# Kernel tuning notes

Hardware: AMD Instinct MI355X
Metric: run time of the kernel (lower is better)

## Reference

```python
import jax, jax.numpy as jnp
import numpy as np

N_DATA = 32768
N_CHK = 32768
N = N_DATA + N_CHK          # 65536 nodes
E = 524288                  # edges (before self-loops)
F_IN = 10                   # node_feature_dim
HID = 128                   # hidden_dim
HEADS = 4
C = HID // HEADS            # 32 per-head channels
L = 4                       # num_gnn_layers
EPS_LN = 1e-5


def layer_norm(x, g, b):
    mu = x.mean(-1, keepdims=True)
    var = ((x - mu) ** 2).mean(-1, keepdims=True)
    return (x - mu) * jax.lax.rsqrt(var + EPS_LN) * g + b


def mlp3(x, W1, b1, W2, b2, W3, b3):
    h = jax.nn.relu(x @ W1 + b1)
    h = jax.nn.relu(h @ W2 + b2)
    return h @ W3 + b3


def setup_inputs() -> dict:
    key = jax.random.key(0)
    ks = jax.random.split(key, 32)
    s = 0.02
    inp = {
        'node_features': jax.random.normal(ks[0], (N, F_IN), jnp.float32),
        'edge_index': jax.random.randint(ks[1], (2, E), 0, N, dtype=jnp.int64),
        # node embedding: Linear(F_IN,HID) + LayerNorm
        'W_emb': s * jax.random.normal(ks[2], (F_IN, HID), jnp.float32),
        'b_emb': jnp.zeros((HID,), jnp.float32),
        'ln0_g': jnp.ones((HID,), jnp.float32),
        'ln0_b': jnp.zeros((HID,), jnp.float32),
        # L GATConv layers (stacked): lin weight, att_src/att_dst, bias, post-LN
        'Wg': s * jax.random.normal(ks[3], (L, HID, HID), jnp.float32),
        'att_s': s * jax.random.normal(ks[4], (L, HEADS, C), jnp.float32),
        'att_d': s * jax.random.normal(ks[5], (L, HEADS, C), jnp.float32),
        'bg': jnp.zeros((L, HID), jnp.float32),
        'lng': jnp.ones((L, HID), jnp.float32),
        'lnb': jnp.zeros((L, HID), jnp.float32),
        # policy net
        'pW1': s * jax.random.normal(ks[6], (HID, HID), jnp.float32),
        'pb1': jnp.zeros((HID,), jnp.float32),
        'pW2': s * jax.random.normal(ks[7], (HID, HID // 2), jnp.float32),
        'pb2': jnp.zeros((HID // 2,), jnp.float32),
        'pW3': s * jax.random.normal(ks[8], (HID // 2, 2), jnp.float32),
        'pb3': jnp.zeros((2,), jnp.float32),
        # value net
        'vW1': s * jax.random.normal(ks[9], (HID, HID), jnp.float32),
        'vb1': jnp.zeros((HID,), jnp.float32),
        'vW2': s * jax.random.normal(ks[10], (HID, HID // 2), jnp.float32),
        'vb2': jnp.zeros((HID // 2,), jnp.float32),
        'vW3': s * jax.random.normal(ks[11], (HID // 2, 1), jnp.float32),
        'vb3': jnp.zeros((1,), jnp.float32),
    }
    return inp


def reference(node_features, edge_index, W_emb, b_emb, ln0_g, ln0_b,
              Wg, att_s, att_d, bg, lng, lnb,
              pW1, pb1, pW2, pb2, pW3, pb3,
              vW1, vb1, vW2, vb2, vW3, vb3):
    n = node_features.shape[0]
    # PyG GATConv adds self-loops by default
    loops = jnp.arange(n, dtype=edge_index.dtype)
    ei = jnp.concatenate([edge_index, jnp.stack([loops, loops])], axis=1)
    src, dst = ei[0], ei[1]

    # node embedding (dropout is identity in eval)
    x = jax.nn.relu(layer_norm(node_features @ W_emb + b_emb, ln0_g, ln0_b))

    for l in range(L):
        h = (x @ Wg[l]).reshape(n, HEADS, C)                       # [N,H,C]
        a_s = jnp.einsum('nhc,hc->nh', h, att_s[l])                # [N,H]
        a_d = jnp.einsum('nhc,hc->nh', h, att_d[l])
        alpha = jax.nn.leaky_relu(a_s[src] + a_d[dst], 0.2)        # [E+N,H]
        # segment softmax over destination node per head
        m = jax.ops.segment_max(alpha, dst, num_segments=n)
        alpha = jnp.exp(alpha - m[dst])
        denom = jax.ops.segment_sum(alpha, dst, num_segments=n)
        alpha = alpha / (denom[dst] + 1e-16)
        out = jax.ops.segment_sum(alpha[:, :, None] * h[src], dst,
                                  num_segments=n)                  # [N,H,C]
        out = out.reshape(n, HID) + bg[l]
        x = layer_norm(x + jax.nn.relu(out), lng[l], lnb[l])

    logits = mlp3(x[:N_DATA], pW1, pb1, pW2, pb2, pW3, pb3)        # [N_DATA,2]
    pooled = x.mean(axis=0, keepdims=True)                         # [1,HID]
    value = mlp3(pooled, vW1, vb1, vW2, vb2, vW3, vb3)             # [1,1]
    return logits, value
```

## Files before the change

kernel.cpp:

```cpp
#include <hip/hip_runtime.h>

#define NNODES 65536
#define NDATA  32768
#define HID    128
#define HEADS  4
#define CHANS  32
#define LAYERS 4

using bf16x8 = __attribute__((ext_vector_type(8))) short;
using f32x4  = __attribute__((ext_vector_type(4))) float;

__device__ __forceinline__ float wave_reduce_sum(float v) {
#pragma unroll
    for (int m = 1; m < 64; m <<= 1) v += __shfl_xor(v, m, 64);
    return v;
}

__device__ __forceinline__ unsigned short bf16_rne(float f) {
    unsigned u = __float_as_uint(f);
    return (unsigned short)((u + 0x7fffu + ((u >> 16) & 1u)) >> 16);
}
__device__ __forceinline__ float bf2f(unsigned short u) {
    return __uint_as_float((unsigned)u << 16);
}

__device__ __forceinline__ void gload_lds16(const unsigned short* g, unsigned short* l) {
    __builtin_amdgcn_global_load_lds(
        (const __attribute__((address_space(1))) void*)g,
        (__attribute__((address_space(3))) void*)l, 16, 0, 0);
}

__global__ void hist_kernel(const int* __restrict__ ei, int* __restrict__ deg, int Eo) {
    int e = blockIdx.x * 256 + threadIdx.x;
    if (e >= Eo) return;
    atomicAdd(&deg[ei[Eo + e]], 1);
}

__global__ void scan1(const int* __restrict__ deg, int* __restrict__ offs, int* __restrict__ bsum) {
    __shared__ int s[256];
    int t = threadIdx.x, b = blockIdx.x;
    int v = deg[b * 256 + t] + 1;
    s[t] = v;
    __syncthreads();
    for (int off = 1; off < 256; off <<= 1) {
        int add = (t >= off) ? s[t - off] : 0;
        __syncthreads();
        s[t] += add;
        __syncthreads();
    }
    offs[b * 256 + t] = s[t] - v;
    if (t == 255) bsum[b] = s[255];
}

__global__ void scan2(int* __restrict__ bsum) {
    __shared__ int s[256];
    int t = threadIdx.x;
    int v = bsum[t];
    s[t] = v;
    __syncthreads();
    for (int off = 1; off < 256; off <<= 1) {
        int add = (t >= off) ? s[t - off] : 0;
        __syncthreads();
        s[t] += add;
        __syncthreads();
    }
    bsum[t] = s[t] - v;
}

__global__ void scan3(int* __restrict__ offs, const int* __restrict__ bsum,
                      int* __restrict__ cursor, int Eo) {
    int i = blockIdx.x * 256 + threadIdx.x;
    int v = offs[i] + bsum[i >> 8];
    offs[i] = v;
    cursor[i] = v;
    if (i == 0) offs[NNODES] = Eo + NNODES;
}

__global__ void fill_kernel(const int* __restrict__ ei, int* __restrict__ cursor,
                            int* __restrict__ col, int Eo) {
    int e = blockIdx.x * 256 + threadIdx.x;
    int Etot = Eo + NNODES;
    if (e >= Etot) return;
    int src, dst;
    if (e < Eo) { src = ei[e]; dst = ei[Eo + e]; }
    else        { src = dst = e - Eo; }
    int pos = atomicAdd(&cursor[dst], 1);
    col[pos] = src;
}

__global__ void prep_all(const float* __restrict__ Wg, const float* __restrict__ attS,
                         const float* __restrict__ attD,
                         const float* __restrict__ pW1, const float* __restrict__ pW2,
                         const float* __restrict__ vW1, const float* __restrict__ vW2,
                         unsigned short* __restrict__ wh, unsigned short* __restrict__ wl,
                         unsigned short* __restrict__ w1h, unsigned short* __restrict__ w1l,
                         unsigned short* __restrict__ w2h, unsigned short* __restrict__ w2l,
                         float* __restrict__ w1t, float* __restrict__ w2t)
{
    int id = blockIdx.x * 256 + threadIdx.x;
    if (id < 4 * 144 * 128) {
        int l = id / (144 * 128);
        int rem = id % (144 * 128);
        int n = rem / 128, k = rem % 128;
        const float* W = Wg + (size_t)l * HID * HID;
        float v = 0.f;
        if (n < 128) {
            v = W[k * HID + n];
        } else if (n < 136) {
            int h = (n - 128) & 3;
            const float* av = ((n - 128) < 4 ? attS : attD) + l * HID + h * CHANS;
            for (int c = 0; c < CHANS; c++) v += W[k * HID + h * CHANS + c] * av[c];
        }
        unsigned short hh = bf16_rne(v);
        int t = n >> 4, bcol = n & 15;
        int ks = k >> 5, kq = (k >> 3) & 3, e = k & 7;
        size_t o = (size_t)l * (144 * 128) + (size_t)(((t * 4 + ks) * 64) + (kq * 16 + bcol)) * 8 + e;
        wh[o] = hh;
        wl[o] = bf16_rne(v - bf2f(hh));
        return;
    }
    id -= 4 * 144 * 128;
    if (id < 24576) {
        int n, k;
        float v;
        unsigned short *dh, *dl;
        if (id < 16384) {
            n = id / 128; k = id % 128;
            v = pW1[k * 128 + n];
            dh = w1h; dl = w1l;
        } else {
            int j = id - 16384;
            n = j / 128; k = j % 128;
            v = pW2[k * 64 + n];
            dh = w2h; dl = w2l;
        }
        unsigned short hh = bf16_rne(v);
        int t = n >> 4, bcol = n & 15;
        int ks = k >> 5, kq = (k >> 3) & 3, e = k & 7;
        size_t o = (size_t)(((t * 4 + ks) * 64) + (kq * 16 + bcol)) * 8 + e;
        dh[o] = hh;
        dl[o] = bf16_rne(v - bf2f(hh));
        return;
    }
    id -= 24576;
    if (id < 16384) {
        int t = id >> 7, k = id & 127;
        w1t[t * 128 + k] = vW1[k * 128 + t];
    } else if (id < 24576) {
        int j = id - 16384;
        int t = j >> 7, k = j & 127;
        w2t[t * 128 + k] = vW2[k * 64 + t];
    }
}

__global__ __launch_bounds__(256) void embed_kernel(
    const float* __restrict__ feat, const float* __restrict__ W,
    const float* __restrict__ bb, const float* __restrict__ g,
    const float* __restrict__ be, unsigned short* __restrict__ xh,
    unsigned short* __restrict__ xl)
{
    int node = blockIdx.x * 4 + (threadIdx.x >> 6);
    int lane = threadIdx.x & 63;
    float f[10];
#pragma unroll
    for (int i = 0; i < 10; i++) f[i] = feat[node * 10 + i];
    int c0 = 2 * lane, c1 = c0 + 1;
    float v0 = bb[c0], v1 = bb[c1];
#pragma unroll
    for (int i = 0; i < 10; i++) {
        v0 = fmaf(f[i], W[i * HID + c0], v0);
        v1 = fmaf(f[i], W[i * HID + c1], v1);
    }
    float mu = wave_reduce_sum(v0 + v1) * (1.f / 128.f);
    float e0 = v0 - mu, e1 = v1 - mu;
    float var = wave_reduce_sum(e0 * e0 + e1 * e1) * (1.f / 128.f);
    float r = 1.f / sqrtf(var + 1e-5f);
    float r0 = fmaxf(e0 * r * g[c0] + be[c0], 0.f);
    float r1 = fmaxf(e1 * r * g[c1] + be[c1], 0.f);
    unsigned short h0 = bf16_rne(r0), h1 = bf16_rne(r1);
    unsigned short l0 = bf16_rne(r0 - bf2f(h0)), l1 = bf16_rne(r1 - bf2f(h1));
    size_t xi = (size_t)node * HID;
    *(unsigned*)(xh + xi + c0) = (unsigned)h0 | ((unsigned)h1 << 16);
    *(unsigned*)(xl + xi + c0) = (unsigned)l0 | ((unsigned)l1 << 16);
}

template <int NT, int EPI>
__global__ __launch_bounds__(512, 4) void mfma_gemm(
    const unsigned short* __restrict__ Ah,
    const unsigned short* __restrict__ Bh, const unsigned short* __restrict__ Bl,
    const float* __restrict__ bias,
    unsigned short* __restrict__ outH,
    float* __restrict__ a_s, float* __restrict__ a_d,
    const float* __restrict__ wfin, const float* __restrict__ bfin,
    float* __restrict__ outF)
{
    __shared__ unsigned short lds[NT * 2048];

    int tid = threadIdx.x;
    int wid = tid >> 6, l = tid & 63;
    int row = blockIdx.x * 128 + wid * 16 + (l & 15);
    int kg = (l >> 4) * 8;

    const unsigned short* arh = Ah + (size_t)row * 128 + kg;
    bf16x8 afh[4];
#pragma unroll
    for (int ks = 0; ks < 4; ks++) afh[ks] = *(const bf16x8*)(arh + ks * 32);

    f32x4 acc[NT];
#pragma unroll
    for (int t = 0; t < NT; t++) acc[t] = (f32x4){0.f, 0.f, 0.f, 0.f};

#pragma unroll
    for (int p = 0; p < 2; p++) {
        __syncthreads();
        for (int c = wid; c < 4 * NT; c += 8) {
            int fr = c >> 1, lo = c & 1;
            int t = fr >> 1, ksl = fr & 1;
            const unsigned short* src = (lo ? Bl : Bh)
                + ((size_t)(t * 4 + p * 2 + ksl) << 9) + ((unsigned)l << 3);
            gload_lds16(src, &lds[(size_t)c << 9]);
        }
        __syncthreads();
#pragma unroll
        for (int ksl = 0; ksl < 2; ksl++) {
            int ks = p * 2 + ksl;
#pragma unroll
            for (int t = 0; t < NT; t++) {
                const unsigned short* bp = &lds[(((t * 2 + ksl) << 1) << 9) + (l << 3)];
                bf16x8 bh  = *(const bf16x8*)bp;
                bf16x8 blo = *(const bf16x8*)(bp + 512);
                acc[t] = __builtin_amdgcn_mfma_f32_16x16x32_bf16(afh[ks], bh,  acc[t], 0, 0, 0);
                acc[t] = __builtin_amdgcn_mfma_f32_16x16x32_bf16(afh[ks], blo, acc[t], 0, 0, 0);
            }
        }
    }

    int ecol = l & 15;
    int er0 = blockIdx.x * 128 + wid * 16 + ((l >> 4) << 2);

    if constexpr (EPI == 0) {
#pragma unroll
        for (int t = 0; t < 8; t++)
#pragma unroll
            for (int j = 0; j < 4; j++)
                outH[(size_t)(er0 + j) * 128 + t * 16 + ecol] = bf16_rne(acc[t][j]);
#pragma unroll
        for (int j = 0; j < 4; j++) {
            float v = acc[8][j];
            if (ecol < 4)      a_s[(er0 + j) * 4 + ecol] = v;
            else if (ecol < 8) a_d[(er0 + j) * 4 + (ecol - 4)] = v;
        }
    } else if constexpr (EPI == 1) {
#pragma unroll
        for (int t = 0; t < NT; t++)
#pragma unroll
            for (int j = 0; j < 4; j++) {
                float v = fmaxf(acc[t][j] + bias[t * 16 + ecol], 0.f);
                outH[(size_t)(er0 + j) * 128 + t * 16 + ecol] = bf16_rne(v);
            }
    } else {
        float p0[4], p1[4];
#pragma unroll
        for (int j = 0; j < 4; j++) { p0[j] = 0.f; p1[j] = 0.f; }
#pragma unroll
        for (int t = 0; t < NT; t++) {
            int cc = t * 16 + ecol;
            float w0 = wfin[cc * 2 + 0], w1 = wfin[cc * 2 + 1];
#pragma unroll
            for (int j = 0; j < 4; j++) {
                float v = fmaxf(acc[t][j] + bias[cc], 0.f);
                p0[j] = fmaf(v, w0, p0[j]);
                p1[j] = fmaf(v, w1, p1[j]);
            }
        }
#pragma unroll
        for (int m = 1; m < 16; m <<= 1)
#pragma unroll
            for (int j = 0; j < 4; j++) {
                p0[j] += __shfl_xor(p0[j], m, 64);
                p1[j] += __shfl_xor(p1[j], m, 64);
            }
        if (ecol == 0) {
            float b0 = bfin[0], b1 = bfin[1];
#pragma unroll
            for (int j = 0; j < 4; j++) {
                outF[(er0 + j) * 2 + 0] = p0[j] + b0;
                outF[(er0 + j) * 2 + 1] = p1[j] + b1;
            }
        }
    }
}

__global__ __launch_bounds__(256) void gat_agg(
    const unsigned short* __restrict__ hb, const float* __restrict__ a_s,
    const float* __restrict__ a_d, const int* __restrict__ offs,
    const int* __restrict__ col, const float* __restrict__ bgl,
    const float* __restrict__ gl, const float* __restrict__ bl,
    unsigned short* __restrict__ xh, unsigned short* __restrict__ xl)
{
    __shared__ int2 whs[4][4][64];
    int wv = threadIdx.x >> 6;
    int lane = threadIdx.x & 63;
    int node = blockIdx.x * 4 + wv;
    int s = offs[node], e = offs[node + 1];
    int deg = e - s;
    float4 ad = *(const float4*)(a_d + (size_t)node * 4);

    int c0 = 2 * lane, c1 = 2 * lane + 1;
    int head = lane >> 4;
    float acc0 = 0.f, acc1 = 0.f;
    float den = 1e-16f;

    if (deg <= 64) {
        int src = 0;
        float e0 = 0.f, e1 = 0.f, e2 = 0.f, e3 = 0.f;
        if (lane < deg) {
            src = col[s + lane];
            float4 as = *(const float4*)(a_s + (size_t)src * 4);
            float s0 = as.x + ad.x; s0 = fmaxf(s0, 0.2f * s0);
            float s1 = as.y + ad.y; s1 = fmaxf(s1, 0.2f * s1);
            float s2 = as.z + ad.z; s2 = fmaxf(s2, 0.2f * s2);
            float s3 = as.w + ad.w; s3 = fmaxf(s3, 0.2f * s3);
            e0 = __expf(s0); e1 = __expf(s1); e2 = __expf(s2); e3 = __expf(s3);
        }
        whs[wv][0][lane] = make_int2(__float_as_int(e0), src);
        whs[wv][1][lane] = make_int2(__float_as_int(e1), src);
        whs[wv][2][lane] = make_int2(__float_as_int(e2), src);
        whs[wv][3][lane] = make_int2(__float_as_int(e3), src);
        const int2* wrow = &whs[wv][head][0];
        int dg4 = (deg + 3) & ~3;
        for (int j = 0; j < dg4; j += 4) {
            int2 q0 = wrow[j + 0], q1 = wrow[j + 1];
            int2 q2 = wrow[j + 2], q3 = wrow[j + 3];
            float w0 = __int_as_float(q0.x), w1 = __int_as_float(q1.x);
            float w2 = __int_as_float(q2.x), w3 = __int_as_float(q3.x);
            unsigned v0 = *(const unsigned*)(hb + (((unsigned)q0.y << 7) + (unsigned)c0));
            unsigned v1 = *(const unsigned*)(hb + (((unsigned)q1.y << 7) + (unsigned)c0));
            unsigned v2 = *(const unsigned*)(hb + (((unsigned)q2.y << 7) + (unsigned)c0));
            unsigned v3 = *(const unsigned*)(hb + (((unsigned)q3.y << 7) + (unsigned)c0));
            den += (w0 + w1) + (w2 + w3);
            acc0 = fmaf(w0, __uint_as_float(v0 << 16), acc0);
            acc1 = fmaf(w0, __uint_as_float(v0 & 0xffff0000u), acc1);
            acc0 = fmaf(w1, __uint_as_float(v1 << 16), acc0);
            acc1 = fmaf(w1, __uint_as_float(v1 & 0xffff0000u), acc1);
            acc0 = fmaf(w2, __uint_as_float(v2 << 16), acc0);
            acc1 = fmaf(w2, __uint_as_float(v2 & 0xffff0000u), acc1);
            acc0 = fmaf(w3, __uint_as_float(v3 << 16), acc0);
            acc1 = fmaf(w3, __uint_as_float(v3 & 0xffff0000u), acc1);
        }
    } else {
        for (int j = s; j < e; j++) {
            int src = col[j];
            float4 as = *(const float4*)(a_s + (size_t)src * 4);
            float sh = (head == 0) ? (as.x + ad.x) : (head == 1) ? (as.y + ad.y)
                     : (head == 2) ? (as.z + ad.z) : (as.w + ad.w);
            sh = fmaxf(sh, 0.2f * sh);
            float wj = __expf(sh);
            den += wj;
            unsigned hv = *(const unsigned*)(hb + (((unsigned)src << 7) + (unsigned)c0));
            acc0 = fmaf(wj, __uint_as_float(hv << 16), acc0);
            acc1 = fmaf(wj, __uint_as_float(hv & 0xffff0000u), acc1);
        }
    }
    float inv = 1.f / den;
    acc0 *= inv;
    acc1 *= inv;

    float o0 = fmaxf(acc0 + bgl[c0], 0.f);
    float o1 = fmaxf(acc1 + bgl[c1], 0.f);
    size_t xi = (size_t)node * HID;
    unsigned ph = *(const unsigned*)(xh + xi + c0);
    unsigned pl = *(const unsigned*)(xl + xi + c0);
    float x0 = __uint_as_float(ph << 16) + __uint_as_float(pl << 16);
    float x1 = __uint_as_float(ph & 0xffff0000u) + __uint_as_float(pl & 0xffff0000u);
    float t0 = x0 + o0, t1 = x1 + o1;
    float mu = wave_reduce_sum(t0 + t1) * (1.f / 128.f);
    float e0 = t0 - mu, e1 = t1 - mu;
    float var = wave_reduce_sum(e0 * e0 + e1 * e1) * (1.f / 128.f);
    float r = 1.f / sqrtf(var + 1e-5f);
    float r0 = e0 * r * gl[c0] + bl[c0];
    float r1 = e1 * r * gl[c1] + bl[c1];
    unsigned short h0 = bf16_rne(r0), h1 = bf16_rne(r1);
    unsigned short l0 = bf16_rne(r0 - bf2f(h0)), l1 = bf16_rne(r1 - bf2f(h1));
    *(unsigned*)(xh + xi + c0) = (unsigned)h0 | ((unsigned)h1 << 16);
    *(unsigned*)(xl + xi + c0) = (unsigned)l0 | ((unsigned)l1 << 16);
}

__global__ void pool_sum(const unsigned short* __restrict__ xh,
                         const unsigned short* __restrict__ xl, float* __restrict__ partial) {
    int t = threadIdx.x;
    int base = blockIdx.x * 256;
    float s = 0.f;
    for (int i = 0; i < 256; i++) {
        size_t idx = (size_t)(base + i) * HID + t;
        s += bf2f(xh[idx]) + bf2f(xl[idx]);
    }
    partial[blockIdx.x * 128 + t] = s;
}

__global__ void value_mlp(const float* __restrict__ partial,
                          const float* __restrict__ w1t, const float* __restrict__ b1,
                          const float* __restrict__ w2t, const float* __restrict__ b2,
                          const float* __restrict__ W3, const float* __restrict__ b3,
                          float* __restrict__ out)
{
    __shared__ float p[128], h1[128], h2[64];
    int t = threadIdx.x;
    float s = 0.f;
    for (int i = 0; i < 256; i++) s += partial[i * 128 + t];
    p[t] = s * (1.f / (float)NNODES);
    __syncthreads();
    float a = b1[t];
    const float4* wr = (const float4*)(w1t + (size_t)t * 128);
#pragma unroll
    for (int k4 = 0; k4 < 32; k4++) {
        float4 w = wr[k4];
        a += p[4 * k4] * w.x + p[4 * k4 + 1] * w.y + p[4 * k4 + 2] * w.z + p[4 * k4 + 3] * w.w;
    }
    h1[t] = fmaxf(a, 0.f);
    __syncthreads();
    if (t < 64) {
        float a2 = b2[t];
        const float4* wr2 = (const float4*)(w2t + (size_t)t * 128);
#pragma unroll
        for (int k4 = 0; k4 < 32; k4++) {
            float4 w = wr2[k4];
            a2 += h1[4 * k4] * w.x + h1[4 * k4 + 1] * w.y + h1[4 * k4 + 2] * w.z + h1[4 * k4 + 3] * w.w;
        }
        h2[t] = fmaxf(a2, 0.f);
    }
    __syncthreads();
    if (t == 0) {
        float v = b3[0];
        for (int k = 0; k < 64; k++) v = fmaf(h2[k], W3[k], v);
        out[NDATA * 2] = v;
    }
}

extern "C" void kernel_launch(void* const* d_in, const int* in_sizes, int n_in,
                              void* d_out, int out_size, void* d_ws, size_t ws_size,
                              hipStream_t stream)
{
    const float* feat  = (const float*)d_in[0];
    const int*   ei    = (const int*)d_in[1];
    const float* W_emb = (const float*)d_in[2];
    const float* b_emb = (const float*)d_in[3];
    const float* ln0g  = (const float*)d_in[4];
    const float* ln0b  = (const float*)d_in[5];
    const float* Wg    = (const float*)d_in[6];
    const float* att_s = (const float*)d_in[7];
    const float* att_d = (const float*)d_in[8];
    const float* bg    = (const float*)d_in[9];
    const float* lng   = (const float*)d_in[10];
    const float* lnb   = (const float*)d_in[11];
    const float* pW1 = (const float*)d_in[12]; const float* pb1 = (const float*)d_in[13];
    const float* pW2 = (const float*)d_in[14]; const float* pb2 = (const float*)d_in[15];
    const float* pW3 = (const float*)d_in[16]; const float* pb3 = (const float*)d_in[17];
    const float* vW1 = (const float*)d_in[18]; const float* vb1 = (const float*)d_in[19];
    const float* vW2 = (const float*)d_in[20]; const float* vb2 = (const float*)d_in[21];
    const float* vW3 = (const float*)d_in[22]; const float* vb3 = (const float*)d_in[23];
    float* out = (float*)d_out;
    int Eo = in_sizes[1] / 2;

    unsigned short* xh = (unsigned short*)d_ws;
    unsigned short* xl = xh + (size_t)NNODES * HID;
    unsigned short* hb = xl + (size_t)NNODES * HID;
    float* a_s = (float*)(hb + (size_t)NNODES * HID);
    float* a_d = a_s + NNODES * HEADS;
    unsigned short* wgt_h = (unsigned short*)(a_d + NNODES * HEADS);
    unsigned short* wgt_l = wgt_h + 4 * 144 * 128;
    unsigned short* pw1h  = wgt_l + 4 * 144 * 128;
    unsigned short* pw1l  = pw1h + 128 * 128;
    unsigned short* pw2h  = pw1l + 128 * 128;
    unsigned short* pw2l  = pw2h + 64 * 128;
    float* w1t  = (float*)(pw2l + 64 * 128);
    float* w2t  = w1t + 128 * 128;
    float* partial = w2t + 64 * 128;
    int* deg    = (int*)(partial + 256 * 128);
    int* offs   = deg + NNODES;
    int* cursor = offs + NNODES + 2;
    int* bsum   = cursor + NNODES;
    int* col    = bsum + 256;
    unsigned short* ph1h = hb;

    prep_all<<<(4 * 144 * 128 + 24576 + 24576) / 256, 256, 0, stream>>>(
        Wg, att_s, att_d, pW1, pW2, vW1, vW2,
        wgt_h, wgt_l, pw1h, pw1l, pw2h, pw2l, w1t, w2t);

    hipMemsetAsync(deg, 0, (size_t)NNODES * 4, stream);
    hist_kernel<<<(Eo + 255) / 256, 256, 0, stream>>>(ei, deg, Eo);
    scan1<<<256, 256, 0, stream>>>(deg, offs, bsum);
    scan2<<<1, 256, 0, stream>>>(bsum);
    scan3<<<256, 256, 0, stream>>>(offs, bsum, cursor, Eo);
    fill_kernel<<<(Eo + NNODES + 255) / 256, 256, 0, stream>>>(ei, cursor, col, Eo);

    embed_kernel<<<NNODES / 4, 256, 0, stream>>>(feat, W_emb, b_emb, ln0g, ln0b, xh, xl);

    for (int l = 0; l < LAYERS; l++) {
        mfma_gemm<9, 0><<<NNODES / 128, 512, 0, stream>>>(
            xh, wgt_h + (size_t)l * 144 * 128, wgt_l + (size_t)l * 144 * 128,
            nullptr, hb, a_s, a_d, nullptr, nullptr, nullptr);
        gat_agg<<<NNODES / 4, 256, 0, stream>>>(
            hb, a_s, a_d, offs, col, bg + l * HID, lng + l * HID, lnb + l * HID, xh, xl);
    }

    mfma_gemm<8, 1><<<NDATA / 128, 512, 0, stream>>>(
        xh, pw1h, pw1l, pb1, ph1h, nullptr, nullptr, nullptr, nullptr, nullptr);
    mfma_gemm<4, 2><<<NDATA / 128, 512, 0, stream>>>(
        ph1h, pw2h, pw2l, pb2, nullptr, nullptr, nullptr, pW3, pb3, out);

    pool_sum<<<256, 128, 0, stream>>>(xh, xl, partial);
    value_mlp<<<1, 128, 0, stream>>>(partial, w1t, vb1, w2t, vb2, vW3, vb3, out);
}
```

Measured before the change: 348.6 us.

## Drop low-bf16 residual storage, fuse embed into prep, merge scan kernels

Node activations are now kept only as a single bf16 array. The low-order residual array xl, along with its reads and writes in gat_agg, embed and pool_sum, is removed, which cuts memory traffic per layer. The embedding kernel is folded into the weight-prep launch, and the separate scan2 block-sum kernel is replaced by a per-block wave reduction inside scan3, removing two launches. In exchange, the residual path and LayerNorm inputs lose precision because they are rounded to bf16 each layer.

New measurement: 330.6 us. 5.2% less time.

```diff
diff --git a/kernel.cpp b/kernel.cpp
--- a/kernel.cpp
+++ b/kernel.cpp
@@ -11,6 +11,12 @@
 using f32x4  = __attribute__((ext_vector_type(4))) float;
 
 __device__ __forceinline__ float wave_reduce_sum(float v) {
+#pragma unroll
+    for (int m = 1; m < 64; m <<= 1) v += __shfl_xor(v, m, 64);
+    return v;
+}
+
+__device__ __forceinline__ int wave_reduce_sum_i(int v) {
 #pragma unroll
     for (int m = 1; m < 64; m <<= 1) v += __shfl_xor(v, m, 64);
     return v;
@@ -52,27 +58,19 @@
     if (t == 255) bsum[b] = s[255];
 }
 
-__global__ void scan2(int* __restrict__ bsum) {
-    __shared__ int s[256];
-    int t = threadIdx.x;
-    int v = bsum[t];
-    s[t] = v;
-    __syncthreads();
-    for (int off = 1; off < 256; off <<= 1) {
-        int add = (t >= off) ? s[t - off] : 0;
-        __syncthreads();
-        s[t] += add;
-        __syncthreads();
-    }
-    bsum[t] = s[t] - v;
-}
-
 __global__ void scan3(int* __restrict__ offs, const int* __restrict__ bsum,
                       int* __restrict__ cursor, int Eo) {
-    int i = blockIdx.x * 256 + threadIdx.x;
-    int v = offs[i] + bsum[i >> 8];
-    offs[i] = v;
-    cursor[i] = v;
+    __shared__ int ws[4];
+    int b = blockIdx.x, t = threadIdx.x;
+    int v = (t < b) ? bsum[t] : 0;
+    v = wave_reduce_sum_i(v);
+    if ((t & 63) == 0) ws[t >> 6] = v;
+    __syncthreads();
+    int base = ws[0] + ws[1] + ws[2] + ws[3];
+    int i = b * 256 + t;
+    int o = offs[i] + base;
+    offs[i] = o;
+    cursor[i] = o;
     if (i == 0) offs[NNODES] = Eo + NNODES;
 }
 
@@ -88,16 +86,43 @@
     col[pos] = src;
 }
 
-__global__ void prep_all(const float* __restrict__ Wg, const float* __restrict__ attS,
-                         const float* __restrict__ attD,
-                         const float* __restrict__ pW1, const float* __restrict__ pW2,
-                         const float* __restrict__ vW1, const float* __restrict__ vW2,
-                         unsigned short* __restrict__ wh, unsigned short* __restrict__ wl,
-                         unsigned short* __restrict__ w1h, unsigned short* __restrict__ w1l,
-                         unsigned short* __restrict__ w2h, unsigned short* __restrict__ w2l,
-                         float* __restrict__ w1t, float* __restrict__ w2t)
+__global__ __launch_bounds__(256) void prep_embed(
+    const float* __restrict__ feat, const float* __restrict__ W_emb,
+    const float* __restrict__ b_emb, const float* __restrict__ ln0g,
+    const float* __restrict__ ln0b, unsigned short* __restrict__ xh,
+    const float* __restrict__ Wg, const float* __restrict__ attS,
+    const float* __restrict__ attD,
+    const float* __restrict__ pW1, const float* __restrict__ pW2,
+    const float* __restrict__ vW1, const float* __restrict__ vW2,
+    unsigned short* __restrict__ wh, unsigned short* __restrict__ wl,
+    unsigned short* __restrict__ w1h, unsigned short* __restrict__ w1l,
+    unsigned short* __restrict__ w2h, unsigned short* __restrict__ w2l,
+    float* __restrict__ w1t, float* __restrict__ w2t)
 {
-    int id = blockIdx.x * 256 + threadIdx.x;
+    if (blockIdx.x < NNODES / 4) {
+        int node = blockIdx.x * 4 + (threadIdx.x >> 6);
+        int lane = threadIdx.x & 63;
+        float f[10];
+#pragma unroll
+        for (int i = 0; i < 10; i++) f[i] = feat[node * 10 + i];
+        int c0 = 2 * lane, c1 = c0 + 1;
+        float v0 = b_emb[c0], v1 = b_emb[c1];
+#pragma unroll
+        for (int i = 0; i < 10; i++) {
+            v0 = fmaf(f[i], W_emb[i * HID + c0], v0);
+            v1 = fmaf(f[i], W_emb[i * HID + c1], v1);
+        }
+        float mu = wave_reduce_sum(v0 + v1) * (1.f / 128.f);
+        float e0 = v0 - mu, e1 = v1 - mu;
+        float var = wave_reduce_sum(e0 * e0 + e1 * e1) * (1.f / 128.f);
+        float r = 1.f / sqrtf(var + 1e-5f);
+        float r0 = fmaxf(e0 * r * ln0g[c0] + ln0b[c0], 0.f);
+        float r1 = fmaxf(e1 * r * ln0g[c1] + ln0b[c1], 0.f);
+        *(unsigned*)(xh + (size_t)node * HID + c0) =
+            (unsigned)bf16_rne(r0) | ((unsigned)bf16_rne(r1) << 16);
+        return;
+    }
+    int id = (blockIdx.x - NNODES / 4) * 256 + threadIdx.x;
     if (id < 4 * 144 * 128) {
         int l = id / (144 * 128);
         int rem = id % (144 * 128);
@@ -153,37 +178,6 @@
     }
 }
 
-__global__ __launch_bounds__(256) void embed_kernel(
-    const float* __restrict__ feat, const float* __restrict__ W,
-    const float* __restrict__ bb, const float* __restrict__ g,
-    const float* __restrict__ be, unsigned short* __restrict__ xh,
-    unsigned short* __restrict__ xl)
-{
-    int node = blockIdx.x * 4 + (threadIdx.x >> 6);
-    int lane = threadIdx.x & 63;
-    float f[10];
-#pragma unroll
-    for (int i = 0; i < 10; i++) f[i] = feat[node * 10 + i];
-    int c0 = 2 * lane, c1 = c0 + 1;
-    float v0 = bb[c0], v1 = bb[c1];
-#pragma unroll
-    for (int i = 0; i < 10; i++) {
-        v0 = fmaf(f[i], W[i * HID + c0], v0);
-        v1 = fmaf(f[i], W[i * HID + c1], v1);
-    }
-    float mu = wave_reduce_sum(v0 + v1) * (1.f / 128.f);
-    float e0 = v0 - mu, e1 = v1 - mu;
-    float var = wave_reduce_sum(e0 * e0 + e1 * e1) * (1.f / 128.f);
-    float r = 1.f / sqrtf(var + 1e-5f);
-    float r0 = fmaxf(e0 * r * g[c0] + be[c0], 0.f);
-    float r1 = fmaxf(e1 * r * g[c1] + be[c1], 0.f);
-    unsigned short h0 = bf16_rne(r0), h1 = bf16_rne(r1);
-    unsigned short l0 = bf16_rne(r0 - bf2f(h0)), l1 = bf16_rne(r1 - bf2f(h1));
-    size_t xi = (size_t)node * HID;
-    *(unsigned*)(xh + xi + c0) = (unsigned)h0 | ((unsigned)h1 << 16);
-    *(unsigned*)(xl + xi + c0) = (unsigned)l0 | ((unsigned)l1 << 16);
-}
-
 template <int NT, int EPI>
 __global__ __launch_bounds__(512, 4) void mfma_gemm(
     const unsigned short* __restrict__ Ah,
@@ -296,7 +290,7 @@
     const float* __restrict__ a_d, const int* __restrict__ offs,
     const int* __restrict__ col, const float* __restrict__ bgl,
     const float* __restrict__ gl, const float* __restrict__ bl,
-    unsigned short* __restrict__ xh, unsigned short* __restrict__ xl)
+    unsigned short* __restrict__ xh)
 {
     __shared__ int2 whs[4][4][64];
     int wv = threadIdx.x >> 6;
@@ -370,31 +364,23 @@
     float o1 = fmaxf(acc1 + bgl[c1], 0.f);
     size_t xi = (size_t)node * HID;
     unsigned ph = *(const unsigned*)(xh + xi + c0);
-    unsigned pl = *(const unsigned*)(xl + xi + c0);
-    float x0 = __uint_as_float(ph << 16) + __uint_as_float(pl << 16);
-    float x1 = __uint_as_float(ph & 0xffff0000u) + __uint_as_float(pl & 0xffff0000u);
-    float t0 = x0 + o0, t1 = x1 + o1;
+    float t0 = __uint_as_float(ph << 16) + o0;
+    float t1 = __uint_as_float(ph & 0xffff0000u) + o1;
     float mu = wave_reduce_sum(t0 + t1) * (1.f / 128.f);
     float e0 = t0 - mu, e1 = t1 - mu;
     float var = wave_reduce_sum(e0 * e0 + e1 * e1) * (1.f / 128.f);
     float r = 1.f / sqrtf(var + 1e-5f);
     float r0 = e0 * r * gl[c0] + bl[c0];
     float r1 = e1 * r * gl[c1] + bl[c1];
-    unsigned short h0 = bf16_rne(r0), h1 = bf16_rne(r1);
-    unsigned short l0 = bf16_rne(r0 - bf2f(h0)), l1 = bf16_rne(r1 - bf2f(h1));
-    *(unsigned*)(xh + xi + c0) = (unsigned)h0 | ((unsigned)h1 << 16);
-    *(unsigned*)(xl + xi + c0) = (unsigned)l0 | ((unsigned)l1 << 16);
-}
-
-__global__ void pool_sum(const unsigned short* __restrict__ xh,
-                         const unsigned short* __restrict__ xl, float* __restrict__ partial) {
+    *(unsigned*)(xh + xi + c0) = (unsigned)bf16_rne(r0) | ((unsigned)bf16_rne(r1) << 16);
+}
+
+__global__ void pool_sum(const unsigned short* __restrict__ xh, float* __restrict__ partial) {
     int t = threadIdx.x;
     int base = blockIdx.x * 256;
     float s = 0.f;
-    for (int i = 0; i < 256; i++) {
-        size_t idx = (size_t)(base + i) * HID + t;
-        s += bf2f(xh[idx]) + bf2f(xl[idx]);
-    }
+    for (int i = 0; i < 256; i++)
+        s += bf2f(xh[(size_t)(base + i) * HID + t]);
     partial[blockIdx.x * 128 + t] = s;
 }
 
@@ -463,8 +449,7 @@
     int Eo = in_sizes[1] / 2;
 
     unsigned short* xh = (unsigned short*)d_ws;
-    unsigned short* xl = xh + (size_t)NNODES * HID;
-    unsigned short* hb = xl + (size_t)NNODES * HID;
+    unsigned short* hb = xh + (size_t)NNODES * HID;
     float* a_s = (float*)(hb + (size_t)NNODES * HID);
     float* a_d = a_s + NNODES * HEADS;
     unsigned short* wgt_h = (unsigned short*)(a_d + NNODES * HEADS);
@@ -483,25 +468,23 @@
     int* col    = bsum + 256;
     unsigned short* ph1h = hb;
 
-    prep_all<<<(4 * 144 * 128 + 24576 + 24576) / 256, 256, 0, stream>>>(
+    prep_embed<<<NNODES / 4 + 480, 256, 0, stream>>>(
+        feat, W_emb, b_emb, ln0g, ln0b, xh,
         Wg, att_s, att_d, pW1, pW2, vW1, vW2,
         wgt_h, wgt_l, pw1h, pw1l, pw2h, pw2l, w1t, w2t);
 
     hipMemsetAsync(deg, 0, (size_t)NNODES * 4, stream);
     hist_kernel<<<(Eo + 255) / 256, 256, 0, stream>>>(ei, deg, Eo);
     scan1<<<256, 256, 0, stream>>>(deg, offs, bsum);
-    scan2<<<1, 256, 0, stream>>>(bsum);
     scan3<<<256, 256, 0, stream>>>(offs, bsum, cursor, Eo);
     fill_kernel<<<(Eo + NNODES + 255) / 256, 256, 0, stream>>>(ei, cursor, col, Eo);
-
-    embed_kernel<<<NNODES / 4, 256, 0, stream>>>(feat, W_emb, b_emb, ln0g, ln0b, xh, xl);
 
     for (int l = 0; l < LAYERS; l++) {
         mfma_gemm<9, 0><<<NNODES / 128, 512, 0, stream>>>(
             xh, wgt_h + (size_t)l * 144 * 128, wgt_l + (size_t)l * 144 * 128,
             nullptr, hb, a_s, a_d, nullptr, nullptr, nullptr);
         gat_agg<<<NNODES / 4, 256, 0, stream>>>(
-            hb, a_s, a_d, offs, col, bg + l * HID, lng + l * HID, lnb + l * HID, xh, xl);
+            hb, a_s, a_d, offs, col, bg + l * HID, lng + l * HID, lnb + l * HID, xh);
     }
 
     mfma_gemm<8, 1><<<NDATA / 128, 512, 0, stream>>>(
@@ -509,6 +492,6 @@
     mfma_gemm<4, 2><<<NDATA / 128, 512, 0, stream>>>(
         ph1h, pw2h, pw2l, pb2, nullptr, nullptr, nullptr, pW3, pb3, out);
 
-    pool_sum<<<256, 128, 0, stream>>>(xh, xl, partial);
+    pool_sum<<<256, 128, 0, stream>>>(xh, partial);
     value_mlp<<<1, 128, 0, stream>>>(partial, w1t, vb1, w2t, vb2, vW3, vb3, out);
 }
```
